# Performance work log

Hardware: AMD Instinct MI355X
Metric: run time of the kernel (lower is better)

Reference implementation:

```python
import jax, jax.numpy as jnp
import numpy as np
from jax import lax

C, H, W = 512, 4, 4          # channel, height, width (size=[512,4,4])
SPLIT, PRED = 4, 4
WC = W // SPLIT              # width of each chunk = 1
L = C * H * WC               # lstm_size = 2048
B = 16


def setup_inputs() -> dict:
    key = jax.random.key(0)
    ks = jax.random.split(key, 12)
    s = 0.02  # ~1/sqrt(L), keeps gates in a sane range
    def w(k, shape):
        return jax.random.normal(k, shape, jnp.float32) * s
    return {
        "x1": jax.random.normal(ks[0], (B, C, H, W), jnp.float32),
        "x2": jax.random.normal(ks[1], (B, C, H, W), jnp.float32),
        "enc_Wih": w(ks[2], (2, 4 * L, L)),
        "enc_Whh": w(ks[3], (2, 4 * L, L)),
        "enc_bih": w(ks[4], (2, 4 * L)),
        "enc_bhh": w(ks[5], (2, 4 * L)),
        "dec_Wih": w(ks[6], (2, 4 * L, L)),
        "dec_Whh": w(ks[7], (2, 4 * L, L)),
        "dec_bih": w(ks[8], (2, 4 * L)),
        "dec_bhh": w(ks[9], (2, 4 * L)),
        "conv_W": w(ks[10], (C, 2 * C)),
        "conv_b": w(ks[11], (C,)),
    }


def _lstm2(x, state, Wih, Whh, bih, bhh):
    """One time-step of a 2-layer torch-style LSTM. x: [B, L]."""
    h, c = state  # each [2, B, L]
    hs, cs = [], []
    inp = x
    for l in range(2):
        g = inp @ Wih[l].T + bih[l] + h[l] @ Whh[l].T + bhh[l]  # [B, 4L]
        i, f, gg, o = jnp.split(g, 4, axis=-1)  # torch gate order i,f,g,o
        cn = jax.nn.sigmoid(f) * c[l] + jax.nn.sigmoid(i) * jnp.tanh(gg)
        hn = jax.nn.sigmoid(o) * jnp.tanh(cn)
        hs.append(hn); cs.append(cn)
        inp = hn
    return inp, (jnp.stack(hs), jnp.stack(cs))


def _split_chunks(x, reverse_inside=False):
    # torch.stack(torch.split(x, WC, dim=3)).view(SPLIT, -1, 1, L)
    b = x.shape[0]
    a = x.reshape(b, C, H, SPLIT, WC)
    if reverse_inside:
        a = a[..., ::-1]  # flip(dims=[4]) on the stacked chunks
    a = jnp.moveaxis(a, 3, 0)  # [SPLIT, B, C, H, WC]
    return a.reshape(SPLIT, b, L)


def _assemble(chunks, b, flip_inside=False):
    # chunks: [K, B, L] -> image block [B, C, H, K*WC] (width-concat order = chunk order)
    k = chunks.shape[0]
    a = chunks.reshape(k, b, C, H, WC)
    if flip_inside:
        a = a[..., ::-1]  # per-chunk flip(dims=[3]) in the torch code
    a = jnp.transpose(a, (1, 2, 3, 0, 4))
    return a.reshape(b, C, H, k * WC)


def _forward(x1, x2, enc_Wih, enc_Whh, enc_bih, enc_bhh,
             dec_Wih, dec_Whh, dec_bih, dec_bhh, conv_W, conv_b):
    b = x1.shape[0]
    z = jnp.zeros((2, b, L), x1.dtype)
    init = (z, z)

    def enc_step(st, x):
        out, st2 = _lstm2(x, st, enc_Wih, enc_Whh, enc_bih, enc_bhh)
        return st2, out

    def dec_step(st, x):
        out, st2 = _lstm2(x, st, dec_Wih, dec_Whh, dec_bih, dec_bhh)
        return st2, out

    def dec_ar(x0, st, n):
        def step(carry, _):
            x, s = carry
            out, s2 = _lstm2(x, s, dec_Wih, dec_Whh, dec_bih, dec_bhh)
            return (out, s2), out
        _, outs = lax.scan(step, (x0, st), None, length=n)
        return outs  # [n, B, L]

    x1_split = _split_chunks(x1)
    x1_split_rev = _split_chunks(x1, reverse_inside=True)
    x2_split = _split_chunks(x2)
    x2_split_rev = _split_chunks(x2, reverse_inside=True)

    # encoder: forward over x2 chunks; backward over internally-flipped x1 chunks
    hidden_x2, _ = lax.scan(enc_step, init, x2_split)
    hidden_x1r, _ = lax.scan(enc_step, init, x1_split_rev[::-1])

    st1, outs1 = lax.scan(dec_step, hidden_x2, x1_split)
    de1 = outs1[-1]
    preds1 = dec_ar(de1, st1, PRED + SPLIT - 1)  # 7 steps
    extra1 = _assemble(jnp.concatenate([de1[None], preds1], 0), b)
    x1_full = jnp.concatenate([x1, extra1], axis=3)  # width 3*W

    # decoder branch 2: consume reversed x2 chunks from hidden_x1r, prepend outputs
    st2, outs2 = lax.scan(dec_step, hidden_x1r, x2_split_rev[::-1])
    de2 = outs2[-1]
    preds2 = dec_ar(de2, st2, PRED + SPLIT - 1)
    # each output is prepended, so the last prediction ends up at the front
    extra2 = _assemble(jnp.concatenate([preds2[::-1], de2[None]], 0), b, flip_inside=True)
    x2_full = jnp.concatenate([extra2, x2], axis=3)

    x1_parts = (x1_full[..., :W], x1_full[..., W:-W], x1_full[..., -W:])
    x2_parts = (x2_full[..., :W], x2_full[..., W:-W], x2_full[..., -W:])

    mid = jnp.concatenate([x1_parts[1], x2_parts[1]], axis=1)  # [B, 2C, H, W]
    out = jnp.einsum('oi,bihw->bohw', conv_W, mid) + conv_b[None, :, None, None]
    out = jax.nn.leaky_relu(out, 0.2)  # make_layers: 1x1 conv + LeakyReLU
    return out, x1_parts, x2_parts


def reference(x1, x2, enc_Wih, enc_Whh, enc_bih, enc_bhh,
              dec_Wih, dec_Whh, dec_bih, dec_bhh, conv_W, conv_b):
    out, p1, p2 = _forward(x1, x2, enc_Wih, enc_Whh, enc_bih, enc_bhh,
                           dec_Wih, dec_Whh, dec_bih, dec_bhh, conv_W, conv_b)
    return (out,) + p1 + p2
```

## Files before the change

kernel.cpp:

```cpp
#include <hip/hip_runtime.h>
#include <cstdint>
#include <cstddef>


typedef __attribute__((ext_vector_type(8))) short short8;
typedef __attribute__((ext_vector_type(4))) short short4v;
typedef __attribute__((ext_vector_type(4))) float f32x4;

#define NBATCH 16
#define MAT_B   16777216ull
#define WSCALE  64.0f
#define INVWS   (1.0f / 64.0f)

__device__ __forceinline__ short f2bf(float f) {
    union { float f; unsigned u; } c; c.f = f;
    unsigned u = c.u;
    unsigned r = (u + 0x7FFFu + ((u >> 16) & 1u)) >> 16;
    return (short)r;
}

__device__ __forceinline__ uint32_t f4_to_fp8x4(float a, float b, float c, float d) {
    int p = __builtin_amdgcn_cvt_pk_fp8_f32(a, b, 0, false);
    p = __builtin_amdgcn_cvt_pk_fp8_f32(c, d, p, true);
    return (uint32_t)p;
}

__device__ __forceinline__ uint8_t f2fp8hw(float x) {
    return (uint8_t)(__builtin_amdgcn_cvt_pk_fp8_f32(x, x, 0, false) & 0xFF);
}

__device__ __forceinline__ float sigmoidf_(float x) { return 1.f / (1.f + __expf(-x)); }

__device__ __forceinline__ int apos(int n, int k) {
    return ((k >> 5) << 9) + ((((k >> 3) & 3) << 4) + n) * 8 + (k & 7);
}

__global__ __launch_bounds__(256) void k_pack8(
    const float* __restrict__ enc_Wih, const float* __restrict__ enc_Whh,
    const float* __restrict__ dec_Wih, const float* __restrict__ dec_Whh,
    uint8_t* __restrict__ dstbase)
{
    __shared__ uint8_t lbuf[16 * 1032];

    const int blk  = blockIdx.x;
    const int om   = blk >> 10;
    const int mat  = (om + 4) & 7;
    const int sub  = blk & 1023;
    const int bt   = sub >> 1;
    const int half = sub & 1;
    const int tid  = threadIdx.x;

    const float* srcs[4] = { enc_Wih, enc_Whh, dec_Wih, dec_Whh };
    const float* src = srcs[mat >> 1] + (size_t)(mat & 1) * 16777216ull;
    uint8_t* dst = dstbase + (size_t)mat * MAT_B
                 + (((size_t)bt * 64 + half * 32) << 9);

#pragma unroll 4
    for (int it = 0; it < 16; ++it) {
        int s  = it * 256 + tid;
        int rl = s >> 8;
        int c0 = (s & 255) * 4;
        int row = (rl >> 2) * 2048 + bt * 4 + (rl & 3);
        f32x4 v = __builtin_nontemporal_load(
            (const f32x4*)(src + (size_t)row * 2048 + half * 1024 + c0));
        uint32_t w32 = f4_to_fp8x4(v[0] * WSCALE, v[1] * WSCALE,
                                   v[2] * WSCALE, v[3] * WSCALE);
        *(uint32_t*)(lbuf + rl * 1032 + c0) = w32;
    }
    __syncthreads();

#pragma unroll 4
    for (int it = 0; it < 16; ++it) {
        int s    = it * 256 + tid;
        int fl   = s >> 7;
        int w    = s & 127;
        int lane = w >> 1;
        int j0   = (s & 1) * 4;
        int rl   = lane & 15;
        int c0   = fl * 32 + (lane >> 4) * 8 + j0;
        *(uint32_t*)(dst + (size_t)s * 4) = *(const uint32_t*)(lbuf + rl * 1032 + c0);
    }
}

__global__ __launch_bounds__(256) void k_packc(const float* __restrict__ Wc,
                                               short* __restrict__ Wcp)
{
    __shared__ short lb[16 * 1032];
    const int mt = blockIdx.x, tid = threadIdx.x;
#pragma unroll 4
    for (int it = 0; it < 16; ++it) {
        int s = it * 256 + tid;
        int rl = s >> 8;
        int c0 = (s & 255) * 4;
        f32x4 v = *(const f32x4*)(Wc + (size_t)(mt * 16 + rl) * 1024 + c0);
        short4v o;
        o[0] = f2bf(v[0]); o[1] = f2bf(v[1]); o[2] = f2bf(v[2]); o[3] = f2bf(v[3]);
        *(short4v*)(lb + rl * 1032 + c0) = o;
    }
    __syncthreads();
    short* dst = Wcp + (size_t)mt * 16384;
#pragma unroll 4
    for (int it = 0; it < 16; ++it) {
        int s    = it * 256 + tid;
        int fl   = s >> 7;
        int w    = s & 127;
        int lane = w >> 1;
        int j0   = (s & 1) * 4;
        int rl   = lane & 15;
        int c0   = fl * 32 + (lane >> 4) * 8 + j0;
        *(short4v*)(dst + (size_t)s * 4) = *(const short4v*)(lb + rl * 1032 + c0);
    }
}

__global__ __launch_bounds__(256) void k_init(
    const float* __restrict__ x1, const float* __restrict__ x2,
    uint8_t* __restrict__ xc1, uint8_t* __restrict__ xc2,
    uint8_t* __restrict__ hbuf, float* __restrict__ cst,
    float* __restrict__ out)
{
    int i = blockIdx.x * blockDim.x + threadIdx.x;
    cst[i] = 0.f;
    if (i < 65536) { hbuf[i] = 0; hbuf[131072 + i] = 0; }
    if (i < 32768) {
        int b = i >> 11, l = i & 2047;
        f32x4 v1 = ((const f32x4*)x1)[i];
        f32x4 v2 = ((const f32x4*)x2)[i];
        int p = apos(b, l);
        uint32_t q1 = f4_to_fp8x4(v1[0], v1[1], v1[2], v1[3]);
        uint32_t q2 = f4_to_fp8x4(v2[0], v2[1], v2[2], v2[3]);
#pragma unroll
        for (int s = 0; s < 4; ++s) {
            xc1[s * 32768 + p] = (uint8_t)(q1 >> (8 * s));
            xc2[s * 32768 + p] = (uint8_t)(q2 >> (8 * s));
        }
        ((f32x4*)(out + 131072))[i]     = v1;
        ((f32x4*)(out + 6 * 131072))[i] = v2;
    }
}

struct CellJob {
    const uint8_t *Wih, *Whh;
    const float *bih, *bhh;
    const uint8_t *xA, *xB, *hin;
    float *cst;
    uint8_t *hout;
    float *svA, *svB;
    short *midp;
    int slot;
};

__global__ __launch_bounds__(512, 4) void k_cell(CellJob jA, CellJob jB)
{
    __shared__ float gpart[8][2][16][17];

    const CellJob& J = (blockIdx.x < 512) ? jA : jB;
    const int bt   = blockIdx.x & 511;
    const int tid  = threadIdx.x;
    const int w    = tid >> 6;
    const int lane = tid & 63;
    const int r    = lane & 15;
    const int g4   = lane >> 4;
    const int kq   = w & 3;

    const uint8_t* Wsrc = (w < 4) ? J.Wih : J.Whh;
    const uint8_t* uA   = (w < 4) ? J.xA : J.hin;
    const uint8_t* uB   = (w < 4) ? J.xB : (J.hin + 32768);

    const uint8_t* wp = Wsrc + (((size_t)bt * 64 + kq * 16) << 9) + lane * 8;
    const uint8_t* ap = uA + ((kq * 16) << 9) + lane * 8;
    const uint8_t* bp = uB + ((kq * 16) << 9) + lane * 8;

    long wreg[16];
#pragma unroll
    for (int i = 0; i < 16; ++i)
        wreg[i] = *(const long*)(wp + ((size_t)i << 9));

    f32x4 accA = {0.f, 0.f, 0.f, 0.f};
    f32x4 accB = {0.f, 0.f, 0.f, 0.f};
#pragma unroll
    for (int i = 0; i < 16; ++i) {
        long av = *(const long*)(ap + ((size_t)i << 9));
        long bv = *(const long*)(bp + ((size_t)i << 9));
        accA = __builtin_amdgcn_mfma_f32_16x16x32_fp8_fp8(wreg[i], av, accA, 0, 0, 0);
        accB = __builtin_amdgcn_mfma_f32_16x16x32_fp8_fp8(wreg[i], bv, accB, 0, 0, 0);
    }

#pragma unroll
    for (int q = 0; q < 4; ++q) {
        gpart[w][0][g4 * 4 + q][r] = accA[q];
        gpart[w][1][g4 * 4 + q][r] = accB[q];
    }
    __syncthreads();

    if (tid < 128) {
        const int br  = tid >> 6;
        const int chl = (tid >> 4) & 3;
        const int n   = tid & 15;

        float gi = 0.f, gf = 0.f, gg = 0.f, go = 0.f;
#pragma unroll
        for (int ww = 0; ww < 8; ++ww) {
            gi += gpart[ww][br][chl][n];
            gf += gpart[ww][br][4 + chl][n];
            gg += gpart[ww][br][8 + chl][n];
            go += gpart[ww][br][12 + chl][n];
        }
        const int ch = bt * 4 + chl;
        gi = gi * INVWS + J.bih[ch]            + J.bhh[ch];
        gf = gf * INVWS + J.bih[2048 + ch]     + J.bhh[2048 + ch];
        gg = gg * INVWS + J.bih[2 * 2048 + ch] + J.bhh[2 * 2048 + ch];
        go = go * INVWS + J.bih[3 * 2048 + ch] + J.bhh[3 * 2048 + ch];

        const size_t idx = ((size_t)br * NBATCH + n) * 2048 + ch;
        float cold = J.cst[idx];
        float cn = sigmoidf_(gf) * cold + sigmoidf_(gi) * tanhf(gg);
        float hn = sigmoidf_(go) * tanhf(cn);
        J.cst[idx] = cn;
        J.hout[br * 32768 + apos(n, ch)] = f2fp8hw(hn);
        if (br == 0) { if (J.svA) J.svA[(size_t)n * 2048 + ch] = hn; }
        else         { if (J.svB) J.svB[(size_t)n * 2048 + ch] = hn; }
        if (J.midp) {
            int i8, pos;
            if (br == 0) { i8 = ch >> 2;       pos = n * 16 + (ch & 3) * 4 + J.slot; }
            else         { i8 = 512 + (ch >> 2); pos = n * 16 + (ch & 3) * 4 + (3 - J.slot); }
            J.midp[(pos >> 4) * 16384 + (i8 >> 5) * 512
                   + (((i8 >> 3) & 3) * 16 + (pos & 15)) * 8 + (i8 & 7)] = f2bf(hn);
        }
    }
}

__global__ __launch_bounds__(512) void k_outs(const float* __restrict__ SA,
                                              const float* __restrict__ SB,
                                              float* __restrict__ out)
{
    int i  = blockIdx.x * 512 + threadIdx.x;
    int q  = i >> 15;
    int rr = i & 32767;
    const float* base = (q < 2) ? SA : SB;
    int sl0 = (q == 0) ? 0 : (q == 1) ? 4 : (q == 2) ? 7 : 3;
    int stp = (q < 2) ? 1 : -1;
    f32x4 o;
#pragma unroll
    for (int w2 = 0; w2 < 4; ++w2)
        o[w2] = base[(size_t)(sl0 + stp * w2) * 32768 + rr];
    ((f32x4*)(out + (size_t)(2 + q) * 131072))[rr] = o;
}

__global__ __launch_bounds__(256) void k_conv2(const short* __restrict__ Wcp,
                                               const short* __restrict__ midp,
                                               const float* __restrict__ bc,
                                               float* __restrict__ out)
{
    __shared__ float gp[4][16][17];
    const int mt = blockIdx.x >> 4, nt = blockIdx.x & 15;
    const int tid = threadIdx.x, kw = tid >> 6, lane = tid & 63;
    const short* ap = Wcp + (size_t)mt * 16384 + kw * 8 * 512 + lane * 8;
    const short* bp = midp + (size_t)nt * 16384 + kw * 8 * 512 + lane * 8;
    f32x4 acc = {0.f, 0.f, 0.f, 0.f};
#pragma unroll
    for (int i = 0; i < 8; ++i) {
        short8 a = *(const short8*)(ap + i * 512);
        short8 b = *(const short8*)(bp + i * 512);
        acc = __builtin_amdgcn_mfma_f32_16x16x32_bf16(a, b, acc, 0, 0, 0);
    }
    const int r = lane & 15, g4 = lane >> 4;
#pragma unroll
    for (int q = 0; q < 4; ++q) gp[kw][g4 * 4 + q][r] = acc[q];
    __syncthreads();

    const int m = tid >> 4, nl = tid & 15;
    float s = gp[0][m][nl] + gp[1][m][nl] + gp[2][m][nl] + gp[3][m][nl];
    const int o = mt * 16 + m, pos = nt * 16 + nl;
    s += bc[o];
    s = s > 0.f ? s : 0.2f * s;
    const int b = pos >> 4, hp = (pos >> 2) & 3, w = pos & 3;
    out[(size_t)b * 8192 + o * 16 + hp * 4 + w] = s;
}

__global__ void k_wsfail(float* out) { if (threadIdx.x == 0 && blockIdx.x == 0) out[0] = -7.7e7f; }

extern "C" void kernel_launch(void* const* d_in, const int* in_sizes, int n_in,
                              void* d_out, int out_size, void* d_ws, size_t ws_size,
                              hipStream_t stream)
{
    const float* x1      = (const float*)d_in[0];
    const float* x2      = (const float*)d_in[1];
    const float* enc_Wih = (const float*)d_in[2];
    const float* enc_Whh = (const float*)d_in[3];
    const float* enc_bih = (const float*)d_in[4];
    const float* enc_bhh = (const float*)d_in[5];
    const float* dec_Wih = (const float*)d_in[6];
    const float* dec_Whh = (const float*)d_in[7];
    const float* dec_bih = (const float*)d_in[8];
    const float* dec_bhh = (const float*)d_in[9];
    const float* conv_W  = (const float*)d_in[10];
    const float* conv_b  = (const float*)d_in[11];
    float* out = (float*)d_out;

    uint8_t* Wb   = (uint8_t*)d_ws;
    uint8_t* xc1  = Wb + 8 * MAT_B;
    uint8_t* xc2  = xc1 + 131072;
    uint8_t* hbuf = xc2 + 131072;
    float*   cst  = (float*)(hbuf + 262144);
    float*   SA   = cst + 131072;
    float*   SB   = SA + 262144;
    short*   midp = (short*)(SB + 262144);
    short*   Wcp  = midp + 262144;
    size_t need = (size_t)((char*)(Wcp + 524288) - (char*)d_ws);
    if (ws_size < need) { k_wsfail<<<1, 64, 0, stream>>>(out); return; }

    k_init<<<512, 256, 0, stream>>>(x1, x2, xc1, xc2, hbuf, cst, out);
    k_pack8<<<8192, 256, 0, stream>>>(enc_Wih, enc_Whh, dec_Wih, dec_Whh, Wb);
    k_packc<<<32, 256, 0, stream>>>(conv_W, Wcp);

    auto hB = [&](int layer, int par) -> uint8_t* {
        return hbuf + layer * 131072 + par * 65536;
    };

    auto mkJob = [&](int t, int layer) -> CellJob {
        const bool enc = (t <= 4);
        CellJob j;
        int base = enc ? 0 : 4;
        j.Wih = Wb + (size_t)(base + layer) * MAT_B;
        j.Whh = Wb + (size_t)(base + 2 + layer) * MAT_B;
        j.bih = (enc ? enc_bih : dec_bih) + layer * 8192;
        j.bhh = (enc ? enc_bhh : dec_bhh) + layer * 8192;
        if (layer == 0) {
            if (t <= 4)      { j.xA = xc2 + (size_t)(t - 1) * 32768; j.xB = xc1 + (size_t)(4 - t) * 32768; }
            else if (t <= 8) { j.xA = xc1 + (size_t)(t - 5) * 32768; j.xB = xc2 + (size_t)(8 - t) * 32768; }
            else             { const uint8_t* hp = hB(1, (t - 1) & 1); j.xA = hp; j.xB = hp + 32768; }
            j.hin = hB(0, (t - 1) & 1);
            j.cst = cst;
            j.hout = hB(0, t & 1);
            j.svA = nullptr; j.svB = nullptr; j.midp = nullptr; j.slot = 0;
        } else {
            const uint8_t* hx = hB(0, t & 1);
            j.xA = hx; j.xB = hx + 32768;
            j.hin = hB(1, (t - 1) & 1);
            j.cst = cst + 65536;
            j.hout = hB(1, t & 1);
            j.svA = (t >= 8) ? SA + (size_t)(t - 8) * 32768 : nullptr;
            j.svB = (t >= 8) ? SB + (size_t)(t - 8) * 32768 : nullptr;
            j.midp = (t >= 8 && t <= 11) ? midp : nullptr;
            j.slot = (t >= 8) ? (t - 8) : 0;
        }
        return j;
    };

    k_cell<<<512, 512, 0, stream>>>(mkJob(1, 0), mkJob(1, 0));
    for (int t = 2; t <= 8; ++t)
        k_cell<<<1024, 512, 0, stream>>>(mkJob(t, 0), mkJob(t - 1, 1));
    k_cell<<<512, 512, 0, stream>>>(mkJob(8, 1), mkJob(8, 1));
    for (int t = 9; t <= 15; ++t) {
        k_cell<<<512, 512, 0, stream>>>(mkJob(t, 0), mkJob(t, 0));
        k_cell<<<512, 512, 0, stream>>>(mkJob(t, 1), mkJob(t, 1));
    }

    k_outs<<<256, 512, 0, stream>>>(SA, SB, out);
    k_conv2<<<512, 256, 0, stream>>>(Wcp, midp, conv_b, out);
}
```

Measured before the change: 377.2 us.

## Fuse recurrent LSTM steps into one persistent kernel with grid barriers

Result: slower. 1.222 ms (+223.9%).

```diff
diff --git a/kernel.cpp b/kernel.cpp
--- a/kernel.cpp
+++ b/kernel.cpp
@@ -11,6 +11,7 @@
 #define MAT_B   16777216ull
 #define WSCALE  64.0f
 #define INVWS   (1.0f / 64.0f)
+#define NBLK    512
 
 __device__ __forceinline__ short f2bf(float f) {
     union { float f; unsigned u; } c; c.f = f;
@@ -33,6 +34,18 @@
 
 __device__ __forceinline__ int apos(int n, int k) {
     return ((k >> 5) << 9) + ((((k >> 3) & 3) << 4) + n) * 8 + (k & 7);
+}
+
+__device__ __forceinline__ void gbar(unsigned* bar, int idx) {
+    __syncthreads();
+    if (threadIdx.x == 0) {
+        __builtin_amdgcn_fence(__ATOMIC_RELEASE, "agent");
+        __hip_atomic_fetch_add(bar + idx, 1u, __ATOMIC_RELAXED, __HIP_MEMORY_SCOPE_AGENT);
+        while (__hip_atomic_load(bar + idx, __ATOMIC_RELAXED, __HIP_MEMORY_SCOPE_AGENT) < NBLK)
+            __builtin_amdgcn_s_sleep(1);
+        __builtin_amdgcn_fence(__ATOMIC_ACQUIRE, "agent");
+    }
+    __syncthreads();
 }
 
 __global__ __launch_bounds__(256) void k_pack8(
@@ -116,11 +129,12 @@
     const float* __restrict__ x1, const float* __restrict__ x2,
     uint8_t* __restrict__ xc1, uint8_t* __restrict__ xc2,
     uint8_t* __restrict__ hbuf, float* __restrict__ cst,
-    float* __restrict__ out)
+    unsigned* __restrict__ bar, float* __restrict__ out)
 {
     int i = blockIdx.x * blockDim.x + threadIdx.x;
     cst[i] = 0.f;
     if (i < 65536) { hbuf[i] = 0; hbuf[131072 + i] = 0; }
+    if (i < 64) bar[i] = 0u;
     if (i < 32768) {
         int b = i >> 11, l = i & 2047;
         f32x4 v1 = ((const f32x4*)x1)[i];
@@ -138,23 +152,58 @@
     }
 }
 
-struct CellJob {
-    const uint8_t *Wih, *Whh;
-    const float *bih, *bhh;
+struct Ctx {
+    const uint8_t* Wb;
+    const uint8_t* xc1;
+    const uint8_t* xc2;
+    uint8_t* hbuf;
+    float*   cst;
+    float*   SA;
+    float*   SB;
+    short*   midp;
+    const float* enc_bih; const float* enc_bhh;
+    const float* dec_bih; const float* dec_bhh;
+};
+
+__device__ __forceinline__ uint8_t* hB(const Ctx& C, int layer, int par) {
+    return C.hbuf + layer * 131072 + par * 65536;
+}
+
+__device__ void cell_unit(const Ctx& C, int t, int layer,
+                          float (*gpart)[2][16][17])
+{
+    const bool enc = (t <= 4);
+    const int base = enc ? 0 : 4;
+    const uint8_t* Wih = C.Wb + (size_t)(base + layer) * MAT_B;
+    const uint8_t* Whh = C.Wb + (size_t)(base + 2 + layer) * MAT_B;
+    const float* bih = (enc ? C.enc_bih : C.dec_bih) + layer * 8192;
+    const float* bhh = (enc ? C.enc_bhh : C.dec_bhh) + layer * 8192;
+
     const uint8_t *xA, *xB, *hin;
-    float *cst;
-    uint8_t *hout;
-    float *svA, *svB;
-    short *midp;
-    int slot;
-};
-
-__global__ __launch_bounds__(512, 4) void k_cell(CellJob jA, CellJob jB)
-{
-    __shared__ float gpart[8][2][16][17];
-
-    const CellJob& J = (blockIdx.x < 512) ? jA : jB;
-    const int bt   = blockIdx.x & 511;
+    float* cstL; uint8_t* hout;
+    float *svA = nullptr, *svB = nullptr; short* midp = nullptr; int slot = 0;
+    if (layer == 0) {
+        if (t <= 4)      { xA = C.xc2 + (size_t)(t - 1) * 32768; xB = C.xc1 + (size_t)(4 - t) * 32768; }
+        else if (t <= 8) { xA = C.xc1 + (size_t)(t - 5) * 32768; xB = C.xc2 + (size_t)(8 - t) * 32768; }
+        else             { const uint8_t* hp = hB(C, 1, (t - 1) & 1); xA = hp; xB = hp + 32768; }
+        hin = hB(C, 0, (t - 1) & 1);
+        cstL = C.cst;
+        hout = hB(C, 0, t & 1);
+    } else {
+        const uint8_t* hx = hB(C, 0, t & 1);
+        xA = hx; xB = hx + 32768;
+        hin = hB(C, 1, (t - 1) & 1);
+        cstL = C.cst + 65536;
+        hout = hB(C, 1, t & 1);
+        if (t >= 8) {
+            svA = C.SA + (size_t)(t - 8) * 32768;
+            svB = C.SB + (size_t)(t - 8) * 32768;
+            slot = t - 8;
+            if (t <= 11) midp = C.midp;
+        }
+    }
+
+    const int bt   = blockIdx.x;
     const int tid  = threadIdx.x;
     const int w    = tid >> 6;
     const int lane = tid & 63;
@@ -162,13 +211,15 @@
     const int g4   = lane >> 4;
     const int kq   = w & 3;
 
-    const uint8_t* Wsrc = (w < 4) ? J.Wih : J.Whh;
-    const uint8_t* uA   = (w < 4) ? J.xA : J.hin;
-    const uint8_t* uB   = (w < 4) ? J.xB : (J.hin + 32768);
+    const uint8_t* Wsrc = (w < 4) ? Wih : Whh;
+    const uint8_t* uA   = (w < 4) ? xA : hin;
+    const uint8_t* uB   = (w < 4) ? xB : (hin + 32768);
 
     const uint8_t* wp = Wsrc + (((size_t)bt * 64 + kq * 16) << 9) + lane * 8;
     const uint8_t* ap = uA + ((kq * 16) << 9) + lane * 8;
     const uint8_t* bp = uB + ((kq * 16) << 9) + lane * 8;
+
+    __syncthreads();
 
     long wreg[16];
 #pragma unroll
@@ -206,75 +257,95 @@
             go += gpart[ww][br][12 + chl][n];
         }
         const int ch = bt * 4 + chl;
-        gi = gi * INVWS + J.bih[ch]            + J.bhh[ch];
-        gf = gf * INVWS + J.bih[2048 + ch]     + J.bhh[2048 + ch];
-        gg = gg * INVWS + J.bih[2 * 2048 + ch] + J.bhh[2 * 2048 + ch];
-        go = go * INVWS + J.bih[3 * 2048 + ch] + J.bhh[3 * 2048 + ch];
+        gi = gi * INVWS + bih[ch]            + bhh[ch];
+        gf = gf * INVWS + bih[2048 + ch]     + bhh[2048 + ch];
+        gg = gg * INVWS + bih[2 * 2048 + ch] + bhh[2 * 2048 + ch];
+        go = go * INVWS + bih[3 * 2048 + ch] + bhh[3 * 2048 + ch];
 
         const size_t idx = ((size_t)br * NBATCH + n) * 2048 + ch;
-        float cold = J.cst[idx];
+        float cold = cstL[idx];
         float cn = sigmoidf_(gf) * cold + sigmoidf_(gi) * tanhf(gg);
         float hn = sigmoidf_(go) * tanhf(cn);
-        J.cst[idx] = cn;
-        J.hout[br * 32768 + apos(n, ch)] = f2fp8hw(hn);
-        if (br == 0) { if (J.svA) J.svA[(size_t)n * 2048 + ch] = hn; }
-        else         { if (J.svB) J.svB[(size_t)n * 2048 + ch] = hn; }
-        if (J.midp) {
+        cstL[idx] = cn;
+        hout[br * 32768 + apos(n, ch)] = f2fp8hw(hn);
+        if (br == 0) { if (svA) svA[(size_t)n * 2048 + ch] = hn; }
+        else         { if (svB) svB[(size_t)n * 2048 + ch] = hn; }
+        if (midp) {
             int i8, pos;
-            if (br == 0) { i8 = ch >> 2;       pos = n * 16 + (ch & 3) * 4 + J.slot; }
-            else         { i8 = 512 + (ch >> 2); pos = n * 16 + (ch & 3) * 4 + (3 - J.slot); }
-            J.midp[(pos >> 4) * 16384 + (i8 >> 5) * 512
-                   + (((i8 >> 3) & 3) * 16 + (pos & 15)) * 8 + (i8 & 7)] = f2bf(hn);
-        }
-    }
-}
-
-__global__ __launch_bounds__(512) void k_outs(const float* __restrict__ SA,
-                                              const float* __restrict__ SB,
-                                              float* __restrict__ out)
-{
-    int i  = blockIdx.x * 512 + threadIdx.x;
-    int q  = i >> 15;
-    int rr = i & 32767;
-    const float* base = (q < 2) ? SA : SB;
-    int sl0 = (q == 0) ? 0 : (q == 1) ? 4 : (q == 2) ? 7 : 3;
-    int stp = (q < 2) ? 1 : -1;
-    f32x4 o;
-#pragma unroll
-    for (int w2 = 0; w2 < 4; ++w2)
-        o[w2] = base[(size_t)(sl0 + stp * w2) * 32768 + rr];
-    ((f32x4*)(out + (size_t)(2 + q) * 131072))[rr] = o;
-}
-
-__global__ __launch_bounds__(256) void k_conv2(const short* __restrict__ Wcp,
-                                               const short* __restrict__ midp,
-                                               const float* __restrict__ bc,
-                                               float* __restrict__ out)
-{
-    __shared__ float gp[4][16][17];
+            if (br == 0) { i8 = ch >> 2;         pos = n * 16 + (ch & 3) * 4 + slot; }
+            else         { i8 = 512 + (ch >> 2); pos = n * 16 + (ch & 3) * 4 + (3 - slot); }
+            midp[(pos >> 4) * 16384 + (i8 >> 5) * 512
+                 + (((i8 >> 3) & 3) * 16 + (pos & 15)) * 8 + (i8 & 7)] = f2bf(hn);
+        }
+    }
+}
+
+__global__ __launch_bounds__(512, 4) void k_seq(
+    Ctx C, const short* __restrict__ Wcp, const float* __restrict__ conv_b,
+    float* __restrict__ out, unsigned* __restrict__ bar)
+{
+    __shared__ float gpart[8][2][16][17];
+    int nb = 0;
+
+    cell_unit(C, 1, 0, gpart);
+    gbar(bar, nb++);
+    for (int t = 2; t <= 8; ++t) {
+        cell_unit(C, t, 0, gpart);
+        cell_unit(C, t - 1, 1, gpart);
+        gbar(bar, nb++);
+    }
+    cell_unit(C, 8, 1, gpart);
+    gbar(bar, nb++);
+    for (int t = 9; t <= 15; ++t) {
+        cell_unit(C, t, 0, gpart);
+        gbar(bar, nb++);
+        cell_unit(C, t, 1, gpart);
+        gbar(bar, nb++);
+    }
+
+    int gid = blockIdx.x * 512 + threadIdx.x;
+    if (gid < 131072) {
+        int q  = gid >> 15;
+        int rr = gid & 32767;
+        const float* base = (q < 2) ? C.SA : C.SB;
+        int sl0 = (q == 0) ? 0 : (q == 1) ? 4 : (q == 2) ? 7 : 3;
+        int stp = (q < 2) ? 1 : -1;
+        f32x4 o;
+#pragma unroll
+        for (int w2 = 0; w2 < 4; ++w2)
+            o[w2] = base[(size_t)(sl0 + stp * w2) * 32768 + rr];
+        ((f32x4*)(out + (size_t)(2 + q) * 131072))[rr] = o;
+    }
+
+    __syncthreads();
+    float (*gp)[16][17] = (float (*)[16][17])gpart;
+    const int tid = threadIdx.x;
     const int mt = blockIdx.x >> 4, nt = blockIdx.x & 15;
-    const int tid = threadIdx.x, kw = tid >> 6, lane = tid & 63;
-    const short* ap = Wcp + (size_t)mt * 16384 + kw * 8 * 512 + lane * 8;
-    const short* bp = midp + (size_t)nt * 16384 + kw * 8 * 512 + lane * 8;
-    f32x4 acc = {0.f, 0.f, 0.f, 0.f};
-#pragma unroll
-    for (int i = 0; i < 8; ++i) {
-        short8 a = *(const short8*)(ap + i * 512);
-        short8 b = *(const short8*)(bp + i * 512);
-        acc = __builtin_amdgcn_mfma_f32_16x16x32_bf16(a, b, acc, 0, 0, 0);
-    }
-    const int r = lane & 15, g4 = lane >> 4;
-#pragma unroll
-    for (int q = 0; q < 4; ++q) gp[kw][g4 * 4 + q][r] = acc[q];
-    __syncthreads();
-
-    const int m = tid >> 4, nl = tid & 15;
-    float s = gp[0][m][nl] + gp[1][m][nl] + gp[2][m][nl] + gp[3][m][nl];
-    const int o = mt * 16 + m, pos = nt * 16 + nl;
-    s += bc[o];
-    s = s > 0.f ? s : 0.2f * s;
-    const int b = pos >> 4, hp = (pos >> 2) & 3, w = pos & 3;
-    out[(size_t)b * 8192 + o * 16 + hp * 4 + w] = s;
+    if (tid < 256) {
+        const int kw = tid >> 6, lane = tid & 63;
+        const short* ap = Wcp + (size_t)mt * 16384 + kw * 8 * 512 + lane * 8;
+        const short* bp = C.midp + (size_t)nt * 16384 + kw * 8 * 512 + lane * 8;
+        f32x4 acc = {0.f, 0.f, 0.f, 0.f};
+#pragma unroll
+        for (int i = 0; i < 8; ++i) {
+            short8 a = *(const short8*)(ap + i * 512);
+            short8 b = *(const short8*)(bp + i * 512);
+            acc = __builtin_amdgcn_mfma_f32_16x16x32_bf16(a, b, acc, 0, 0, 0);
+        }
+        const int r = lane & 15, g4 = lane >> 4;
+#pragma unroll
+        for (int q = 0; q < 4; ++q) gp[kw][g4 * 4 + q][r] = acc[q];
+    }
+    __syncthreads();
+    if (tid < 256) {
+        const int m = tid >> 4, nl = tid & 15;
+        float s = gp[0][m][nl] + gp[1][m][nl] + gp[2][m][nl] + gp[3][m][nl];
+        const int o = mt * 16 + m, pos = nt * 16 + nl;
+        s += conv_b[o];
+        s = s > 0.f ? s : 0.2f * s;
+        const int b = pos >> 4, hp = (pos >> 2) & 3, w = pos & 3;
+        out[(size_t)b * 8192 + o * 16 + hp * 4 + w] = s;
+    }
 }
 
 __global__ void k_wsfail(float* out) { if (threadIdx.x == 0 && blockIdx.x == 0) out[0] = -7.7e7f; }
@@ -306,56 +377,19 @@
     float*   SB   = SA + 262144;
     short*   midp = (short*)(SB + 262144);
     short*   Wcp  = midp + 262144;
-    size_t need = (size_t)((char*)(Wcp + 524288) - (char*)d_ws);
+    unsigned* bar = (unsigned*)(Wcp + 524288);
+    size_t need = (size_t)((char*)(bar + 64) - (char*)d_ws);
     if (ws_size < need) { k_wsfail<<<1, 64, 0, stream>>>(out); return; }
 
-    k_init<<<512, 256, 0, stream>>>(x1, x2, xc1, xc2, hbuf, cst, out);
+    k_init<<<512, 256, 0, stream>>>(x1, x2, xc1, xc2, hbuf, cst, bar, out);
     k_pack8<<<8192, 256, 0, stream>>>(enc_Wih, enc_Whh, dec_Wih, dec_Whh, Wb);
     k_packc<<<32, 256, 0, stream>>>(conv_W, Wcp);
 
-    auto hB = [&](int layer, int par) -> uint8_t* {
-        return hbuf + layer * 131072 + par * 65536;
-    };
-
-    auto mkJob = [&](int t, int layer) -> CellJob {
-        const bool enc = (t <= 4);
-        CellJob j;
-        int base = enc ? 0 : 4;
-        j.Wih = Wb + (size_t)(base + layer) * MAT_B;
-        j.Whh = Wb + (size_t)(base + 2 + layer) * MAT_B;
-        j.bih = (enc ? enc_bih : dec_bih) + layer * 8192;
-        j.bhh = (enc ? enc_bhh : dec_bhh) + layer * 8192;
-        if (layer == 0) {
-            if (t <= 4)      { j.xA = xc2 + (size_t)(t - 1) * 32768; j.xB = xc1 + (size_t)(4 - t) * 32768; }
-            else if (t <= 8) { j.xA = xc1 + (size_t)(t - 5) * 32768; j.xB = xc2 + (size_t)(8 - t) * 32768; }
-            else             { const uint8_t* hp = hB(1, (t - 1) & 1); j.xA = hp; j.xB = hp + 32768; }
-            j.hin = hB(0, (t - 1) & 1);
-            j.cst = cst;
-            j.hout = hB(0, t & 1);
-            j.svA = nullptr; j.svB = nullptr; j.midp = nullptr; j.slot = 0;
-        } else {
-            const uint8_t* hx = hB(0, t & 1);
-            j.xA = hx; j.xB = hx + 32768;
-            j.hin = hB(1, (t - 1) & 1);
-            j.cst = cst + 65536;
-            j.hout = hB(1, t & 1);
-            j.svA = (t >= 8) ? SA + (size_t)(t - 8) * 32768 : nullptr;
-            j.svB = (t >= 8) ? SB + (size_t)(t - 8) * 32768 : nullptr;
-            j.midp = (t >= 8 && t <= 11) ? midp : nullptr;
-            j.slot = (t >= 8) ? (t - 8) : 0;
-        }
-        return j;
-    };
-
-    k_cell<<<512, 512, 0, stream>>>(mkJob(1, 0), mkJob(1, 0));
-    for (int t = 2; t <= 8; ++t)
-        k_cell<<<1024, 512, 0, stream>>>(mkJob(t, 0), mkJob(t - 1, 1));
-    k_cell<<<512, 512, 0, stream>>>(mkJob(8, 1), mkJob(8, 1));
-    for (int t = 9; t <= 15; ++t) {
-        k_cell<<<512, 512, 0, stream>>>(mkJob(t, 0), mkJob(t, 0));
-        k_cell<<<512, 512, 0, stream>>>(mkJob(t, 1), mkJob(t, 1));
-    }
-
-    k_outs<<<256, 512, 0, stream>>>(SA, SB, out);
-    k_conv2<<<512, 256, 0, stream>>>(Wcp, midp, conv_b, out);
-}
+    Ctx C;
+    C.Wb = Wb; C.xc1 = xc1; C.xc2 = xc2; C.hbuf = hbuf; C.cst = cst;
+    C.SA = SA; C.SB = SB; C.midp = midp;
+    C.enc_bih = enc_bih; C.enc_bhh = enc_bhh;
+    C.dec_bih = dec_bih; C.dec_bhh = dec_bhh;
+
+    k_seq<<<NBLK, 512, 0, stream>>>(C, Wcp, conv_b, out, bar);
+}
```
